# Optimization experiments

Measured on AMD Instinct MI355X. Metric: run time of the kernel, lower is better.

## Reference

```python
import jax, jax.numpy as jnp
import numpy as np

B, N, DIN = 2, 4096, 128
DQK, DV, H = 128, 128, 8
DH = DQK // H  # head dim for q/k
DVH = DV // H  # head dim for v


def setup_inputs() -> dict:
    key = jax.random.key(0)
    ks = jax.random.split(key, 6)
    x = jax.random.normal(ks[0], (B, N, DIN), dtype=jnp.float32)
    # node mask: first batch fully valid, second batch padded to 3/4 length
    lengths = jnp.array([N, 3 * N // 4])
    mask = jnp.arange(N)[None, :] < lengths[:, None]  # [B, N] bool
    # fused q|k|non_att projection (dim_qk*2 + dim_in outputs)
    W1 = jax.random.normal(ks[1], (DIN, DQK * 2 + DIN), dtype=jnp.float32) * (DIN ** -0.5)
    b1 = jnp.zeros((DQK * 2 + DIN,), dtype=jnp.float32)
    Wv = jax.random.normal(ks[2], (DIN, DV), dtype=jnp.float32) * (DIN ** -0.5)
    bv = jnp.zeros((DV,), dtype=jnp.float32)
    Wo = jax.random.normal(ks[3], (DV, DIN), dtype=jnp.float32) * (DV ** -0.5)
    bo = jnp.zeros((DIN,), dtype=jnp.float32)
    return {"x": x, "mask": mask, "W1": W1, "b1": b1, "Wv": Wv, "bv": bv, "Wo": Wo, "bo": bo}


def reference(x, mask, W1, b1, Wv, bv, Wo, bo):
    # x: [B,N,DIN], mask: [B,N] bool (True = valid node)
    m = mask[..., None].astype(x.dtype)  # [B,N,1]
    # fc_1: fused [q | k | non_att], masked like batch_like(..., skip_masking=False)
    h = (x @ W1 + b1) * m  # [B,N,2*DQK+DIN]
    q = h[..., :DQK]
    k = h[..., DQK:2 * DQK]
    non_att = h[..., -DIN:]
    # fc_v, masked
    v = (x @ Wv + bv) * m  # [B,N,DV]
    # multi-head attention coefficients (AttnCoef(1,1)): masked softmax over keys
    qh = q.reshape(B, N, H, DH)
    kh = k.reshape(B, N, H, DH)
    scores = jnp.einsum('bqhd,bkhd->bhqk', qh, kh) / (DH ** 0.5)  # [B,H,N,N]
    neg = jnp.asarray(jnp.finfo(scores.dtype).min, scores.dtype)
    scores = jnp.where(mask[:, None, None, :], scores, neg)
    alpha = jax.nn.softmax(scores, axis=-1)  # [B,H,N,N]
    # apply_attn: per-head weighted sum of v
    vh = v.reshape(B, N, H, DVH)
    att = jnp.einsum('bhqk,bkhd->bqhd', alpha, vh).reshape(B, N, DV)
    # fc_o (dropout p=0 -> identity), masked; add_batch residual with non_att
    out = (att @ Wo + bo) * m
    return (non_att + out) * m
```

## Files before the change

kernel.cpp:

```cpp
#include <hip/hip_runtime.h>
#include <hip/hip_fp16.h>
#include <math.h>

#define BATCH 2
#define SEQ   4096
#define DIN   128
#define NH    8
#define DHD   16
#define MROWS (BATCH * SEQ)
#define QSCALE 0.36067376022224085f

typedef _Float16 h4 __attribute__((ext_vector_type(4)));
typedef _Float16 h8 __attribute__((ext_vector_type(8)));
typedef __fp16   g2 __attribute__((ext_vector_type(2)));
typedef float    f4 __attribute__((ext_vector_type(4)));

typedef union { h8 v; unsigned u[4]; } H8U;

__device__ __forceinline__ int keyperm(int k) {
    return ((k >> 5) & 1) * 32 + ((k >> 2) & 3) * 8 + ((k >> 4) & 1) * 4 + (k & 3);
}

__global__ __launch_bounds__(512) void proj_kernel(
    const float* __restrict__ x, const int* __restrict__ mask,
    const float* __restrict__ W1, const float* __restrict__ Wv,
    const float* __restrict__ b1, const float* __restrict__ bv,
    _Float16* __restrict__ qT, _Float16* __restrict__ kT,
    _Float16* __restrict__ vT4, float* __restrict__ nat)
{
    __shared__ __align__(16) char SMEM[128 * 136 * 2];
    _Float16* Tw  = (_Float16*)SMEM;
    _Float16* T16 = (_Float16*)SMEM;
    float*    T32 = (float*)SMEM;

    const int t = threadIdx.x;
    const int w = t >> 6, lane = t & 63, quad = lane >> 4, mr = lane & 15;
    const int region = blockIdx.x;
    const int row0   = blockIdx.y * 128;
    const int col0   = region * 128;

    if (mask[row0] == 0) return;

    h8 a[4];
    {
        const float* xrow = x + (size_t)(row0 + w * 16 + mr) * 128;
#pragma unroll
        for (int ks = 0; ks < 4; ++ks) {
            const float* xs = xrow + ks * 32 + quad * 8;
            float4 x0 = *reinterpret_cast<const float4*>(xs);
            float4 x1 = *reinterpret_cast<const float4*>(xs + 4);
            h8 av;
            av[0] = (_Float16)x0.x; av[1] = (_Float16)x0.y;
            av[2] = (_Float16)x0.z; av[3] = (_Float16)x0.w;
            av[4] = (_Float16)x1.x; av[5] = (_Float16)x1.y;
            av[6] = (_Float16)x1.z; av[7] = (_Float16)x1.w;
            a[ks] = av;
        }
    }
    {
        const float* wsrc = (region < 3) ? (W1 + col0) : Wv;
        const int wstride = (region < 3) ? 384 : 128;
#pragma unroll
        for (int i = 0; i < 8; ++i) {
            int idx = t + i * 512;
            int k = idx >> 5, c4 = idx & 31;
            float4 v = *reinterpret_cast<const float4*>(wsrc + (size_t)k * wstride + c4 * 4);
            Tw[(c4 * 4 + 0) * 136 + k] = (_Float16)v.x;
            Tw[(c4 * 4 + 1) * 136 + k] = (_Float16)v.y;
            Tw[(c4 * 4 + 2) * 136 + k] = (_Float16)v.z;
            Tw[(c4 * 4 + 3) * 136 + k] = (_Float16)v.w;
        }
    }
    __syncthreads();

    f4 acc[8];
#pragma unroll
    for (int ct = 0; ct < 8; ++ct) {
        f4 ac = {0.f, 0.f, 0.f, 0.f};
#pragma unroll
        for (int ks = 0; ks < 4; ++ks) {
            h8 bb = *reinterpret_cast<const h8*>(
                &Tw[(ct * 16 + mr) * 136 + ks * 32 + quad * 8]);
            ac = __builtin_amdgcn_mfma_f32_16x16x32_f16(a[ks], bb, ac, 0, 0, 0);
        }
        acc[ct] = ac;
    }
    __syncthreads();

    if (region <= 1) {
        float scale = (region == 0) ? QSCALE : 1.0f;
#pragma unroll
        for (int ct = 0; ct < 8; ++ct) {
            float bias = b1[col0 + ct * 16 + mr];
#pragma unroll
            for (int reg = 0; reg < 4; ++reg) {
                int lr = w * 16 + quad * 4 + reg;
                T16[lr * 136 + ct * 16 + mr] =
                    (_Float16)((acc[ct][reg] + bias) * scale);
            }
        }
        __syncthreads();
        _Float16* dstbase = (region == 0) ? qT : kT;
#pragma unroll
        for (int i = 0; i < 4; ++i) {
            int idx = t + i * 512;
            int h = idx >> 8, rr = (idx >> 1) & 127, half = idx & 1;
            *reinterpret_cast<h8*>(
                dstbase + ((size_t)h * MROWS + row0 + rr) * 16 + half * 8) =
                *reinterpret_cast<h8*>(&T16[rr * 136 + h * 16 + half * 8]);
        }
    } else if (region == 2) {
#pragma unroll
        for (int p = 0; p < 2; ++p) {
            __syncthreads();
            if ((w >> 2) == p) {
#pragma unroll
                for (int ct = 0; ct < 8; ++ct) {
                    float bias = b1[256 + ct * 16 + mr];
#pragma unroll
                    for (int reg = 0; reg < 4; ++reg) {
                        int lr = (w & 3) * 16 + quad * 4 + reg;
                        T32[lr * 132 + ct * 16 + mr] = acc[ct][reg] + bias;
                    }
                }
            }
            __syncthreads();
#pragma unroll
            for (int i = 0; i < 4; ++i) {
                int idx = t + i * 512;
                int r = idx >> 5, c4 = idx & 31;
                *reinterpret_cast<float4*>(
                    nat + (size_t)(row0 + p * 64 + r) * 128 + c4 * 4) =
                    *reinterpret_cast<float4*>(&T32[r * 132 + c4 * 4]);
            }
        }
    } else {
#pragma unroll
        for (int ct = 0; ct < 8; ++ct) {
            float bias = bv[ct * 16 + mr];
#pragma unroll
            for (int reg = 0; reg < 4; ++reg) {
                int m = w * 16 + quad * 4 + reg;
                int sub = m >> 6, ml = m & 63;
                T16[(ct * 16 + mr) * 136 + sub * 64 + keyperm(ml)] =
                    (_Float16)(acc[ct][reg] + bias);
            }
        }
        __syncthreads();
#pragma unroll
        for (int i = 0; i < 4; ++i) {
            int idx = t + i * 512;
            int c = idx >> 4, sub = (idx >> 3) & 1, seg = idx & 7;
            int h = c >> 4, d = c & 15;
            int tile = blockIdx.y * 2 + sub;
            *reinterpret_cast<h8*>(
                vT4 + ((size_t)(h * 128 + tile) * 16 + d) * 64 + seg * 8) =
                *reinterpret_cast<h8*>(&T16[c * 136 + sub * 64 + seg * 8]);
        }
    }
}

#define LOADT(K0, K1, K2, K3, V0, V1, TILE)                                   \
    do {                                                                      \
        const _Float16* kp_ = kbase + (size_t)(TILE) * 1024;                  \
        const _Float16* vp_ = vbase + (size_t)(TILE) * 1024;                  \
        K0 = *reinterpret_cast<const h4*>(kp_);                               \
        K1 = *reinterpret_cast<const h4*>(kp_ + 256);                         \
        K2 = *reinterpret_cast<const h4*>(kp_ + 512);                         \
        K3 = *reinterpret_cast<const h4*>(kp_ + 768);                         \
        V0 = *reinterpret_cast<const h8*>(vp_);                               \
        V1 = *reinterpret_cast<const h8*>(vp_ + 32);                          \
    } while (0)

#define PROC_SUB(AQ, K0, K1, K2, K3, V0, V1, O, L)                            \
    do {                                                                      \
        f4 st0 = __builtin_amdgcn_mfma_f32_16x16x16f16(K0, AQ, fzero, 0, 0, 0); \
        f4 st1 = __builtin_amdgcn_mfma_f32_16x16x16f16(K1, AQ, fzero, 0, 0, 0); \
        f4 st2 = __builtin_amdgcn_mfma_f32_16x16x16f16(K2, AQ, fzero, 0, 0, 0); \
        f4 st3 = __builtin_amdgcn_mfma_f32_16x16x16f16(K3, AQ, fzero, 0, 0, 0); \
        H8U pa, pb;                                                           \
        pa.u[0] = __builtin_bit_cast(unsigned, __builtin_amdgcn_cvt_pkrtz(    \
            __builtin_amdgcn_exp2f(st0[0]), __builtin_amdgcn_exp2f(st0[1]))); \
        pa.u[1] = __builtin_bit_cast(unsigned, __builtin_amdgcn_cvt_pkrtz(    \
            __builtin_amdgcn_exp2f(st0[2]), __builtin_amdgcn_exp2f(st0[3]))); \
        pa.u[2] = __builtin_bit_cast(unsigned, __builtin_amdgcn_cvt_pkrtz(    \
            __builtin_amdgcn_exp2f(st1[0]), __builtin_amdgcn_exp2f(st1[1]))); \
        pa.u[3] = __builtin_bit_cast(unsigned, __builtin_amdgcn_cvt_pkrtz(    \
            __builtin_amdgcn_exp2f(st1[2]), __builtin_amdgcn_exp2f(st1[3]))); \
        pb.u[0] = __builtin_bit_cast(unsigned, __builtin_amdgcn_cvt_pkrtz(    \
            __builtin_amdgcn_exp2f(st2[0]), __builtin_amdgcn_exp2f(st2[1]))); \
        pb.u[1] = __builtin_bit_cast(unsigned, __builtin_amdgcn_cvt_pkrtz(    \
            __builtin_amdgcn_exp2f(st2[2]), __builtin_amdgcn_exp2f(st2[3]))); \
        pb.u[2] = __builtin_bit_cast(unsigned, __builtin_amdgcn_cvt_pkrtz(    \
            __builtin_amdgcn_exp2f(st3[0]), __builtin_amdgcn_exp2f(st3[1]))); \
        pb.u[3] = __builtin_bit_cast(unsigned, __builtin_amdgcn_cvt_pkrtz(    \
            __builtin_amdgcn_exp2f(st3[2]), __builtin_amdgcn_exp2f(st3[3]))); \
        O = __builtin_amdgcn_mfma_f32_16x16x32_f16(pa.v, V0, O, 0, 0, 0);     \
        L = __builtin_amdgcn_mfma_f32_16x16x32_f16(pa.v, vones, L, 0, 0, 0);  \
        O = __builtin_amdgcn_mfma_f32_16x16x32_f16(pb.v, V1, O, 0, 0, 0);     \
        L = __builtin_amdgcn_mfma_f32_16x16x32_f16(pb.v, vones, L, 0, 0, 0);  \
    } while (0)

__global__ __launch_bounds__(512) void attn_kernel(
    const _Float16* __restrict__ qT, const _Float16* __restrict__ kT,
    const _Float16* __restrict__ vT4, const int* __restrict__ mask,
    _Float16* __restrict__ att16)
{
    __shared__ float Cmb[4][64][17];

    const int b = blockIdx.z, hh = blockIdx.y, qt = blockIdx.x;
    const int t = threadIdx.x;
    const int w = t >> 6, lane = t & 63, quad = lane >> 4, mr = lane & 15;
    const int wq = w & 3;
    const int g  = w >> 2;
    const int m0 = b * SEQ + qt * 128 + wq * 32;

    if (mask[b * SEQ + qt * 128] == 0) return;

    int tv = mask[b * SEQ + lane * 64];
    const int ntiles = (int)__popcll(__ballot(tv != 0));
    const int half = ntiles >> 1;
    const int tbeg = g ? half : 0;
    const int tend = tbeg + half;

    const h4 aQ0 = *reinterpret_cast<const h4*>(
        qT + ((size_t)hh * MROWS + m0 + mr) * DHD + quad * 4);
    const h4 aQ1 = *reinterpret_cast<const h4*>(
        qT + ((size_t)hh * MROWS + m0 + 16 + mr) * DHD + quad * 4);

    const _Float16* kbase = kT + ((size_t)hh * MROWS + b * SEQ + mr) * DHD + quad * 4;
    const _Float16* vbase = vT4 + ((size_t)(hh * 128 + b * 64) * 16 + mr) * 64 + quad * 8;

    const f4 fzero = {0.f, 0.f, 0.f, 0.f};
    const _Float16 one = (_Float16)1.0f;
    const h8 vones = {one, one, one, one, one, one, one, one};

    h4 ka0, ka1, ka2, ka3, kb0, kb1, kb2, kb3;
    h8 va0, va1, vb0, vb1;
    LOADT(ka0, ka1, ka2, ka3, va0, va1, tbeg);
    LOADT(kb0, kb1, kb2, kb3, vb0, vb1, tbeg + 1);

    f4 O0 = fzero, O1 = fzero, L0 = fzero, L1 = fzero;

    for (int it = tbeg; it < tend; it += 2) {
        PROC_SUB(aQ0, ka0, ka1, ka2, ka3, va0, va1, O0, L0);
        PROC_SUB(aQ1, ka0, ka1, ka2, ka3, va0, va1, O1, L1);
        int nA = (it + 2 < tend) ? (it + 2) : it;
        LOADT(ka0, ka1, ka2, ka3, va0, va1, nA);

        PROC_SUB(aQ0, kb0, kb1, kb2, kb3, vb0, vb1, O0, L0);
        PROC_SUB(aQ1, kb0, kb1, kb2, kb3, vb0, vb1, O1, L1);
        int nB = (it + 3 < tend) ? (it + 3) : (it + 1);
        LOADT(kb0, kb1, kb2, kb3, vb0, vb1, nB);
    }

    if (g == 1) {
#pragma unroll
        for (int reg = 0; reg < 4; ++reg) {
            Cmb[wq][lane][reg]      = O0[reg];
            Cmb[wq][lane][4 + reg]  = O1[reg];
            Cmb[wq][lane][8 + reg]  = L0[reg];
            Cmb[wq][lane][12 + reg] = L1[reg];
        }
    }
    __syncthreads();
    if (g == 0) {
#pragma unroll
        for (int reg = 0; reg < 4; ++reg) {
            float of0 = O0[reg] + Cmb[wq][lane][reg];
            float of1 = O1[reg] + Cmb[wq][lane][4 + reg];
            float lf0 = L0[reg] + Cmb[wq][lane][8 + reg];
            float lf1 = L1[reg] + Cmb[wq][lane][12 + reg];
            att16[(size_t)(m0 + quad * 4 + reg) * 128 + hh * DHD + mr] =
                (_Float16)(of0 / lf0);
            att16[(size_t)(m0 + 16 + quad * 4 + reg) * 128 + hh * DHD + mr] =
                (_Float16)(of1 / lf1);
        }
    }
}

__global__ __launch_bounds__(256) void outproj_kernel(
    const _Float16* __restrict__ att16, const float* __restrict__ Wo,
    const float* __restrict__ nat, const int* __restrict__ mask,
    const float* __restrict__ bo, float* __restrict__ out)
{
    __shared__ __align__(16) _Float16 Tw[64 * 136];

    const int t = threadIdx.x;
    const int w = t >> 6, lane = t & 63, quad = lane >> 4, mr = lane & 15;
    const int row0 = blockIdx.x * 64;
    const int m0 = row0 + w * 16;
    const int c0 = blockIdx.y * 64;

    if (mask[row0] == 0) {
#pragma unroll
        for (int i = 0; i < 4; ++i) {
            int idx = t + i * 256;
            int r = idx >> 4, c4 = idx & 15;
            *reinterpret_cast<float4*>(
                out + (size_t)(row0 + r) * 128 + c0 + c4 * 4) =
                (float4){0.f, 0.f, 0.f, 0.f};
        }
        return;
    }

#pragma unroll
    for (int i = 0; i < 8; ++i) {
        int idx = t + i * 256;
        int k = idx >> 4, c4 = idx & 15;
        float4 v = *reinterpret_cast<const float4*>(Wo + (size_t)k * 128 + c0 + c4 * 4);
        Tw[(c4 * 4 + 0) * 136 + k] = (_Float16)v.x;
        Tw[(c4 * 4 + 1) * 136 + k] = (_Float16)v.y;
        Tw[(c4 * 4 + 2) * 136 + k] = (_Float16)v.z;
        Tw[(c4 * 4 + 3) * 136 + k] = (_Float16)v.w;
    }
    __syncthreads();

    h8 a[4];
#pragma unroll
    for (int ks = 0; ks < 4; ++ks)
        a[ks] = *reinterpret_cast<const h8*>(
            att16 + (size_t)(m0 + mr) * 128 + ks * 32 + quad * 8);

    f4 acc[4];
#pragma unroll
    for (int ct = 0; ct < 4; ++ct) {
        f4 ac = {0.f, 0.f, 0.f, 0.f};
#pragma unroll
        for (int ks = 0; ks < 4; ++ks) {
            h8 bb = *reinterpret_cast<const h8*>(
                &Tw[(ct * 16 + mr) * 136 + ks * 32 + quad * 8]);
            ac = __builtin_amdgcn_mfma_f32_16x16x32_f16(a[ks], bb, ac, 0, 0, 0);
        }
        acc[ct] = ac;
    }

#pragma unroll
    for (int ct = 0; ct < 4; ++ct) {
        float bias = bo[c0 + ct * 16 + mr];
#pragma unroll
        for (int reg = 0; reg < 4; ++reg) {
            int row = m0 + quad * 4 + reg;
            int col = c0 + ct * 16 + mr;
            out[(size_t)row * 128 + col] =
                acc[ct][reg] + bias + nat[(size_t)row * 128 + col];
        }
    }
}

extern "C" void kernel_launch(void* const* d_in, const int* in_sizes, int n_in,
                              void* d_out, int out_size, void* d_ws, size_t ws_size,
                              hipStream_t stream) {
    const float* x    = (const float*)d_in[0];
    const int*   mask = (const int*)  d_in[1];
    const float* W1   = (const float*)d_in[2];
    const float* b1   = (const float*)d_in[3];
    const float* Wv   = (const float*)d_in[4];
    const float* bv   = (const float*)d_in[5];
    const float* Wo   = (const float*)d_in[6];
    const float* bo   = (const float*)d_in[7];
    float* out = (float*)d_out;

    _Float16* qT    = (_Float16*)d_ws;
    _Float16* kT    = qT    + (size_t)NH * MROWS * DHD;
    _Float16* vT4   = kT    + (size_t)NH * MROWS * DHD;
    _Float16* att16 = vT4   + (size_t)DIN * MROWS;
    float*    nat   = (float*)(att16 + (size_t)MROWS * DIN);

    proj_kernel<<<dim3(4, MROWS / 128), 512, 0, stream>>>(
        x, mask, W1, Wv, b1, bv, qT, kT, vT4, nat);
    attn_kernel<<<dim3(SEQ / 128, NH, BATCH), 512, 0, stream>>>(
        qT, kT, vT4, mask, att16);
    outproj_kernel<<<dim3(MROWS / 64, 2), 256, 0, stream>>>(
        att16, Wo, nat, mask, bo, out);
}
```

Before: 128.7 us.

## Store non_att as transposed fp16, coalesce outproj stores, hoist global loads

The non-attention residual is now written by proj_kernel as a column-major fp16 buffer instead of fp32 row-major, which halves its traffic and drops the two-pass fp32 staging. outproj_kernel is split into 32-column tiles (twice the blocks), loads that fp16 residual directly in MFMA register layout, and stages results through shared memory so global stores are coalesced float4 writes. Both kernels now issue their weight and input global loads before doing the fp16 conversion and LDS writes, so the load latencies overlap. Keeping the residual in fp16 adds rounding error to the final output.

```diff
diff --git a/kernel.cpp b/kernel.cpp
--- a/kernel.cpp
+++ b/kernel.cpp
@@ -12,7 +12,6 @@
 
 typedef _Float16 h4 __attribute__((ext_vector_type(4)));
 typedef _Float16 h8 __attribute__((ext_vector_type(8)));
-typedef __fp16   g2 __attribute__((ext_vector_type(2)));
 typedef float    f4 __attribute__((ext_vector_type(4)));
 
 typedef union { h8 v; unsigned u[4]; } H8U;
@@ -26,12 +25,11 @@
     const float* __restrict__ W1, const float* __restrict__ Wv,
     const float* __restrict__ b1, const float* __restrict__ bv,
     _Float16* __restrict__ qT, _Float16* __restrict__ kT,
-    _Float16* __restrict__ vT4, float* __restrict__ nat)
+    _Float16* __restrict__ vT4, _Float16* __restrict__ natT)
 {
     __shared__ __align__(16) char SMEM[128 * 136 * 2];
     _Float16* Tw  = (_Float16*)SMEM;
     _Float16* T16 = (_Float16*)SMEM;
-    float*    T32 = (float*)SMEM;
 
     const int t = threadIdx.x;
     const int w = t >> 6, lane = t & 63, quad = lane >> 4, mr = lane & 15;
@@ -41,35 +39,43 @@
 
     if (mask[row0] == 0) return;
 
-    h8 a[4];
+    const float* wsrc = (region < 3) ? (W1 + col0) : Wv;
+    const int wstride = (region < 3) ? 384 : 128;
+    float4 wv[8];
+#pragma unroll
+    for (int i = 0; i < 8; ++i) {
+        int idx = t + i * 512;
+        int k = idx >> 5, c4 = idx & 31;
+        wv[i] = *reinterpret_cast<const float4*>(wsrc + (size_t)k * wstride + c4 * 4);
+    }
+    float4 xv[8];
     {
         const float* xrow = x + (size_t)(row0 + w * 16 + mr) * 128;
 #pragma unroll
         for (int ks = 0; ks < 4; ++ks) {
-            const float* xs = xrow + ks * 32 + quad * 8;
-            float4 x0 = *reinterpret_cast<const float4*>(xs);
-            float4 x1 = *reinterpret_cast<const float4*>(xs + 4);
-            h8 av;
-            av[0] = (_Float16)x0.x; av[1] = (_Float16)x0.y;
-            av[2] = (_Float16)x0.z; av[3] = (_Float16)x0.w;
-            av[4] = (_Float16)x1.x; av[5] = (_Float16)x1.y;
-            av[6] = (_Float16)x1.z; av[7] = (_Float16)x1.w;
-            a[ks] = av;
-        }
-    }
-    {
-        const float* wsrc = (region < 3) ? (W1 + col0) : Wv;
-        const int wstride = (region < 3) ? 384 : 128;
-#pragma unroll
-        for (int i = 0; i < 8; ++i) {
-            int idx = t + i * 512;
-            int k = idx >> 5, c4 = idx & 31;
-            float4 v = *reinterpret_cast<const float4*>(wsrc + (size_t)k * wstride + c4 * 4);
-            Tw[(c4 * 4 + 0) * 136 + k] = (_Float16)v.x;
-            Tw[(c4 * 4 + 1) * 136 + k] = (_Float16)v.y;
-            Tw[(c4 * 4 + 2) * 136 + k] = (_Float16)v.z;
-            Tw[(c4 * 4 + 3) * 136 + k] = (_Float16)v.w;
-        }
+            xv[2 * ks]     = *reinterpret_cast<const float4*>(xrow + ks * 32 + quad * 8);
+            xv[2 * ks + 1] = *reinterpret_cast<const float4*>(xrow + ks * 32 + quad * 8 + 4);
+        }
+    }
+
+#pragma unroll
+    for (int i = 0; i < 8; ++i) {
+        int idx = t + i * 512;
+        int k = idx >> 5, c4 = idx & 31;
+        Tw[(c4 * 4 + 0) * 136 + k] = (_Float16)wv[i].x;
+        Tw[(c4 * 4 + 1) * 136 + k] = (_Float16)wv[i].y;
+        Tw[(c4 * 4 + 2) * 136 + k] = (_Float16)wv[i].z;
+        Tw[(c4 * 4 + 3) * 136 + k] = (_Float16)wv[i].w;
+    }
+    h8 a[4];
+#pragma unroll
+    for (int ks = 0; ks < 4; ++ks) {
+        h8 av;
+        av[0] = (_Float16)xv[2*ks].x;   av[1] = (_Float16)xv[2*ks].y;
+        av[2] = (_Float16)xv[2*ks].z;   av[3] = (_Float16)xv[2*ks].w;
+        av[4] = (_Float16)xv[2*ks+1].x; av[5] = (_Float16)xv[2*ks+1].y;
+        av[6] = (_Float16)xv[2*ks+1].z; av[7] = (_Float16)xv[2*ks+1].w;
+        a[ks] = av;
     }
     __syncthreads();
 
@@ -111,28 +117,21 @@
         }
     } else if (region == 2) {
 #pragma unroll
-        for (int p = 0; p < 2; ++p) {
-            __syncthreads();
-            if ((w >> 2) == p) {
-#pragma unroll
-                for (int ct = 0; ct < 8; ++ct) {
-                    float bias = b1[256 + ct * 16 + mr];
-#pragma unroll
-                    for (int reg = 0; reg < 4; ++reg) {
-                        int lr = (w & 3) * 16 + quad * 4 + reg;
-                        T32[lr * 132 + ct * 16 + mr] = acc[ct][reg] + bias;
-                    }
-                }
+        for (int ct = 0; ct < 8; ++ct) {
+            float bias = b1[256 + ct * 16 + mr];
+#pragma unroll
+            for (int reg = 0; reg < 4; ++reg) {
+                int m = w * 16 + quad * 4 + reg;
+                T16[(ct * 16 + mr) * 136 + m] = (_Float16)(acc[ct][reg] + bias);
             }
-            __syncthreads();
-#pragma unroll
-            for (int i = 0; i < 4; ++i) {
-                int idx = t + i * 512;
-                int r = idx >> 5, c4 = idx & 31;
-                *reinterpret_cast<float4*>(
-                    nat + (size_t)(row0 + p * 64 + r) * 128 + c4 * 4) =
-                    *reinterpret_cast<float4*>(&T32[r * 132 + c4 * 4]);
-            }
+        }
+        __syncthreads();
+#pragma unroll
+        for (int i = 0; i < 4; ++i) {
+            int idx = t + i * 512;
+            int c = idx >> 4, seg = idx & 15;
+            *reinterpret_cast<h8*>(natT + (size_t)c * MROWS + row0 + seg * 8) =
+                *reinterpret_cast<h8*>(&T16[c * 136 + seg * 8]);
         }
     } else {
 #pragma unroll
@@ -281,22 +280,23 @@
 
 __global__ __launch_bounds__(256) void outproj_kernel(
     const _Float16* __restrict__ att16, const float* __restrict__ Wo,
-    const float* __restrict__ nat, const int* __restrict__ mask,
+    const _Float16* __restrict__ natT, const int* __restrict__ mask,
     const float* __restrict__ bo, float* __restrict__ out)
 {
-    __shared__ __align__(16) _Float16 Tw[64 * 136];
+    __shared__ __align__(16) _Float16 Tw[32 * 136];
+    __shared__ __align__(16) float   To[64 * 36];
 
     const int t = threadIdx.x;
     const int w = t >> 6, lane = t & 63, quad = lane >> 4, mr = lane & 15;
     const int row0 = blockIdx.x * 64;
-    const int m0 = row0 + w * 16;
-    const int c0 = blockIdx.y * 64;
+    const int m0w  = row0 + w * 16;
+    const int c0   = blockIdx.y * 32;
 
     if (mask[row0] == 0) {
 #pragma unroll
-        for (int i = 0; i < 4; ++i) {
+        for (int i = 0; i < 2; ++i) {
             int idx = t + i * 256;
-            int r = idx >> 4, c4 = idx & 15;
+            int r = idx >> 3, c4 = idx & 7;
             *reinterpret_cast<float4*>(
                 out + (size_t)(row0 + r) * 128 + c0 + c4 * 4) =
                 (float4){0.f, 0.f, 0.f, 0.f};
@@ -304,27 +304,37 @@
         return;
     }
 
-#pragma unroll
-    for (int i = 0; i < 8; ++i) {
+    float4 wv[4];
+#pragma unroll
+    for (int i = 0; i < 4; ++i) {
         int idx = t + i * 256;
-        int k = idx >> 4, c4 = idx & 15;
-        float4 v = *reinterpret_cast<const float4*>(Wo + (size_t)k * 128 + c0 + c4 * 4);
-        Tw[(c4 * 4 + 0) * 136 + k] = (_Float16)v.x;
-        Tw[(c4 * 4 + 1) * 136 + k] = (_Float16)v.y;
-        Tw[(c4 * 4 + 2) * 136 + k] = (_Float16)v.z;
-        Tw[(c4 * 4 + 3) * 136 + k] = (_Float16)v.w;
-    }
-    __syncthreads();
-
+        int k = idx >> 3, c4 = idx & 7;
+        wv[i] = *reinterpret_cast<const float4*>(Wo + (size_t)k * 128 + c0 + c4 * 4);
+    }
     h8 a[4];
 #pragma unroll
     for (int ks = 0; ks < 4; ++ks)
         a[ks] = *reinterpret_cast<const h8*>(
-            att16 + (size_t)(m0 + mr) * 128 + ks * 32 + quad * 8);
-
-    f4 acc[4];
-#pragma unroll
-    for (int ct = 0; ct < 4; ++ct) {
+            att16 + (size_t)(m0w + mr) * 128 + ks * 32 + quad * 8);
+    h4 nv[2];
+#pragma unroll
+    for (int ct = 0; ct < 2; ++ct)
+        nv[ct] = *reinterpret_cast<const h4*>(
+            natT + (size_t)(c0 + ct * 16 + mr) * MROWS + m0w + quad * 4);
+#pragma unroll
+    for (int i = 0; i < 4; ++i) {
+        int idx = t + i * 256;
+        int k = idx >> 3, c4 = idx & 7;
+        Tw[(c4 * 4 + 0) * 136 + k] = (_Float16)wv[i].x;
+        Tw[(c4 * 4 + 1) * 136 + k] = (_Float16)wv[i].y;
+        Tw[(c4 * 4 + 2) * 136 + k] = (_Float16)wv[i].z;
+        Tw[(c4 * 4 + 3) * 136 + k] = (_Float16)wv[i].w;
+    }
+    __syncthreads();
+
+    f4 acc[2];
+#pragma unroll
+    for (int ct = 0; ct < 2; ++ct) {
         f4 ac = {0.f, 0.f, 0.f, 0.f};
 #pragma unroll
         for (int ks = 0; ks < 4; ++ks) {
@@ -336,15 +346,22 @@
     }
 
 #pragma unroll
-    for (int ct = 0; ct < 4; ++ct) {
+    for (int ct = 0; ct < 2; ++ct) {
         float bias = bo[c0 + ct * 16 + mr];
 #pragma unroll
         for (int reg = 0; reg < 4; ++reg) {
-            int row = m0 + quad * 4 + reg;
-            int col = c0 + ct * 16 + mr;
-            out[(size_t)row * 128 + col] =
-                acc[ct][reg] + bias + nat[(size_t)row * 128 + col];
-        }
+            int lr = w * 16 + quad * 4 + reg;
+            To[lr * 36 + ct * 16 + mr] = acc[ct][reg] + bias + (float)nv[ct][reg];
+        }
+    }
+    __syncthreads();
+#pragma unroll
+    for (int i = 0; i < 2; ++i) {
+        int idx = t + i * 256;
+        int r = idx >> 3, c4 = idx & 7;
+        *reinterpret_cast<float4*>(
+            out + (size_t)(row0 + r) * 128 + c0 + c4 * 4) =
+            *reinterpret_cast<float4*>(&To[r * 36 + c4 * 4]);
     }
 }
 
@@ -365,12 +382,12 @@
     _Float16* kT    = qT    + (size_t)NH * MROWS * DHD;
     _Float16* vT4   = kT    + (size_t)NH * MROWS * DHD;
     _Float16* att16 = vT4   + (size_t)DIN * MROWS;
-    float*    nat   = (float*)(att16 + (size_t)MROWS * DIN);
+    _Float16* natT  = att16 + (size_t)MROWS * DIN;
 
     proj_kernel<<<dim3(4, MROWS / 128), 512, 0, stream>>>(
-        x, mask, W1, Wv, b1, bv, qT, kT, vT4, nat);
+        x, mask, W1, Wv, b1, bv, qT, kT, vT4, natT);
     attn_kernel<<<dim3(SEQ / 128, NH, BATCH), 512, 0, stream>>>(
         qT, kT, vT4, mask, att16);
-    outproj_kernel<<<dim3(MROWS / 64, 2), 256, 0, stream>>>(
-        att16, Wo, nat, mask, bo, out);
-}
+    outproj_kernel<<<dim3(MROWS / 64, 4), 256, 0, stream>>>(
+        att16, Wo, natT, mask, bo, out);
+}
```

Result: faster. 123.1 us (-4.3%).
